# Optimization experiments

Measured on AMD Instinct MI355X. Metric: run time of the kernel, lower is better.

The kernel has to match this reference:

```python
import jax, jax.numpy as jnp
import numpy as np

N = 50000
E = 1000000
WIDTH = 64
DEPTH = 4


def setup_inputs() -> dict:
    key = jax.random.key(0)
    ks = jax.random.split(key, 6)
    x = jax.random.normal(ks[0], (N, 5), dtype=jnp.float32)
    edge_index = jax.random.randint(ks[1], (2, E), 0, N, dtype=jnp.int32)
    edge_attr = jax.random.normal(ks[2], (E, 3), dtype=jnp.float32)
    w1 = jax.random.normal(ks[3], (3, WIDTH), dtype=jnp.float32) / jnp.sqrt(3.0)
    b1 = jnp.zeros((WIDTH,), jnp.float32)
    w2 = jax.random.normal(ks[4], (WIDTH, 1), dtype=jnp.float32) / jnp.sqrt(float(WIDTH))
    b2 = jnp.zeros((1,), jnp.float32)
    root = jax.random.normal(ks[5], (1, 1), dtype=jnp.float32)
    bias = jnp.zeros((1,), jnp.float32)
    return dict(x=x, edge_index=edge_index, edge_attr=edge_attr,
                w1=w1, b1=b1, w2=w2, b2=b2, root=root, bias=bias)


def reference(x, edge_index, edge_attr, w1, b1, w2, b2, root, bias):
    # h: scalar node feature, column 2 of data.x -> [N, 1]
    h = x[:, 2:3]
    src, dst = edge_index[0], edge_index[1]  # messages flow src -> dst

    # Per-edge 1x1 weight from the edge MLP (depends only on edge_attr,
    # identical for all depth iterations since the conv is shared).
    w_e = jax.nn.relu(edge_attr @ w1 + b1) @ w2 + b2  # [E, 1]

    # Mean aggregation: precompute in-degree of each target node.
    deg = jax.ops.segment_sum(jnp.ones((E,), jnp.float32), dst, num_segments=N)
    inv_deg = jnp.where(deg > 0, 1.0 / jnp.maximum(deg, 1.0), 0.0)[:, None]  # [N, 1]

    for _ in range(DEPTH):
        msg = h[src] * w_e                                        # gather + per-edge weight, [E, 1]
        agg = jax.ops.segment_sum(msg, dst, num_segments=N) * inv_deg  # scatter-mean, [N, 1]
        h = jax.nn.relu(agg + h @ root + bias)                    # root transform + bias + ReLU
    return h
```

## Files before the change

### kernel.cpp

```cpp
#include <hip/hip_runtime.h>

#define NN 50000
#define NE 1000000
#define NBK 196
#define EPB 1024
#define PB 977
#define ESTRIDE 5632
#define RK 12

__global__ void init_fixed(const float* __restrict__ x, float* __restrict__ h,
                           int* __restrict__ cursor, int* __restrict__ sBeg,
                           int* __restrict__ sLim) {
    int i = blockIdx.x * 256 + threadIdx.x;
    if (i < NN) h[i] = x[5 * i + 2];
    if (i < NBK) {
        cursor[i] = i * ESTRIDE;
        sBeg[i]   = i * ESTRIDE;
        sLim[i]   = (i + 1) * ESTRIDE;
    }
}

__global__ void bucket_count(const int* __restrict__ dst, int* __restrict__ bcnt,
                             const float* __restrict__ x, float* __restrict__ h) {
    __shared__ int hist[NBK];
    int t = threadIdx.x;
    if (t < NBK) hist[t] = 0;
    __syncthreads();
    int gid = blockIdx.x * 256 + t;
    if (gid < NN) h[gid] = x[5 * gid + 2];
#pragma unroll
    for (int j = 0; j < 4; ++j) {
        int e = blockIdx.x * EPB + j * 256 + t;
        if (e < NE) atomicAdd(&hist[dst[e] >> 8], 1);
    }
    __syncthreads();
    if (t < NBK && hist[t]) atomicAdd(&bcnt[t], hist[t]);
}

__global__ void bucket_scan(const int* __restrict__ bcnt,
                            int* __restrict__ sBeg,
                            int* __restrict__ cursor,
                            int* __restrict__ sLim) {
    __shared__ int part[256];
    int t = threadIdx.x;
    int v = (t < NBK) ? ((bcnt[t] + 1) & ~1) : 0;
    part[t] = v;
    __syncthreads();
    for (int off = 1; off < 256; off <<= 1) {
        int x = part[t];
        int add = (t >= off) ? part[t - off] : 0;
        __syncthreads();
        part[t] = x + add;
        __syncthreads();
    }
    if (t < NBK) {
        int excl = part[t] - v;
        sBeg[t] = excl;
        cursor[t] = excl;
        sLim[t] = 0x7FFFFFFF;
    }
}

__global__ void place_kernel(const float* __restrict__ ea,
                             const int* __restrict__ src,
                             const int* __restrict__ dst,
                             const float* __restrict__ w1,
                             const float* __restrict__ b1,
                             const float* __restrict__ w2,
                             const float* __restrict__ b2,
                             const int* __restrict__ sLim,
                             int* __restrict__ cursor,
                             uint2* __restrict__ es,
                             int dumpbase) {
    __shared__ float sw1[192];
    __shared__ float sb1[64];
    __shared__ float sw2[64];
    __shared__ float sce[EPB];
    __shared__ int hist[NBK];
    __shared__ int hbase[NBK];
    int t = threadIdx.x;
    if (t < 192) sw1[t] = w1[t];
    if (t < 64) { sb1[t] = b1[t]; sw2[t] = w2[t]; }
    if (t < NBK) hist[t] = 0;
    __syncthreads();

    int r[4], dd[4];
#pragma unroll
    for (int j = 0; j < 4; ++j) {
        int e = blockIdx.x * EPB + j * 256 + t;
        dd[j] = -1;
        if (e < NE) {
            float a0 = ea[3 * e + 0];
            float a1 = ea[3 * e + 1];
            float a2 = ea[3 * e + 2];
            float c0 = b2[0], c1 = 0.f, c2 = 0.f, c3 = 0.f;
#pragma unroll
            for (int k = 0; k < 64; k += 4) {
                float h0 = fmaf(a0, sw1[k+0], fmaf(a1, sw1[64+k+0], fmaf(a2, sw1[128+k+0], sb1[k+0])));
                float h1 = fmaf(a0, sw1[k+1], fmaf(a1, sw1[64+k+1], fmaf(a2, sw1[128+k+1], sb1[k+1])));
                float h2 = fmaf(a0, sw1[k+2], fmaf(a1, sw1[64+k+2], fmaf(a2, sw1[128+k+2], sb1[k+2])));
                float h3 = fmaf(a0, sw1[k+3], fmaf(a1, sw1[64+k+3], fmaf(a2, sw1[128+k+3], sb1[k+3])));
                c0 = fmaf(fmaxf(h0, 0.f), sw2[k+0], c0);
                c1 = fmaf(fmaxf(h1, 0.f), sw2[k+1], c1);
                c2 = fmaf(fmaxf(h2, 0.f), sw2[k+2], c2);
                c3 = fmaf(fmaxf(h3, 0.f), sw2[k+3], c3);
            }
            sce[j * 256 + t] = (c0 + c1) + (c2 + c3);
            int d = dst[e];
            dd[j] = d;
            r[j] = atomicAdd(&hist[d >> 8], 1);
        }
    }
    __syncthreads();
    if (t < NBK) { int hv = hist[t]; if (hv) hbase[t] = atomicAdd(&cursor[t], hv); }
    __syncthreads();
#pragma unroll
    for (int j = 0; j < 4; ++j) {
        int e = blockIdx.x * EPB + j * 256 + t;
        if (e < NE) {
            int d = dd[j];
            int b = d >> 8;
            int pos = hbase[b] + r[j];
            if (pos >= sLim[b]) pos = dumpbase + (t & 63);
            unsigned pack = (unsigned)src[e] | ((unsigned)(d & 255) << 17);
            es[pos] = make_uint2(pack, __float_as_uint(sce[j * 256 + t]));
        }
    }
}

__global__ void round1_slice(const int* __restrict__ sBeg,
                             const int* __restrict__ sEnd,
                             const int* __restrict__ sLim,
                             const uint2* __restrict__ es,
                             const float* __restrict__ hold,
                             float* __restrict__ aggS,
                             int* __restrict__ degS) {
    __shared__ float lagg[256];
    __shared__ int ldeg[256];
    int t = threadIdx.x;
    int b = blockIdx.x / RK, c = blockIdx.x % RK;
    lagg[t] = 0.f;
    ldeg[t] = 0;
    __syncthreads();
    int s0 = sBeg[b];
    int s1 = sEnd[b];
    { int cap = sLim[b]; if (s1 > cap) s1 = cap; }
    const uint4* es4 = (const uint4*)es;
    for (int p = s0 + (c * 256 + t) * 2; p < s1; p += RK * 512) {
        uint4 v = es4[p >> 1];
        {
            int sidx = v.x & 0x1FFFF;
            int dl = (v.x >> 17) & 255;
            atomicAdd(&lagg[dl], hold[sidx] * __uint_as_float(v.y));
            atomicAdd(&ldeg[dl], 1);
        }
        if (p + 1 < s1) {
            int sidx = v.z & 0x1FFFF;
            int dl = (v.z >> 17) & 255;
            atomicAdd(&lagg[dl], hold[sidx] * __uint_as_float(v.w));
            atomicAdd(&ldeg[dl], 1);
        }
    }
    __syncthreads();
    int node = b * 256 + t;
    if (node < NN) {
        aggS[c * NN + node] = lagg[t];
        degS[c * NN + node] = ldeg[t];
    }
}

__global__ void round_slice(const int* __restrict__ sBeg,
                            const int* __restrict__ sEnd,
                            const int* __restrict__ sLim,
                            const uint2* __restrict__ es,
                            const float* __restrict__ hold,
                            float* __restrict__ aggS) {
    __shared__ float lagg[256];
    int t = threadIdx.x;
    int b = blockIdx.x / RK, c = blockIdx.x % RK;
    lagg[t] = 0.f;
    __syncthreads();
    int s0 = sBeg[b];
    int s1 = sEnd[b];
    { int cap = sLim[b]; if (s1 > cap) s1 = cap; }
    const uint4* es4 = (const uint4*)es;
    for (int p = s0 + (c * 256 + t) * 2; p < s1; p += RK * 512) {
        uint4 v = es4[p >> 1];
        {
            int sidx = v.x & 0x1FFFF;
            int dl = (v.x >> 17) & 255;
            atomicAdd(&lagg[dl], hold[sidx] * __uint_as_float(v.y));
        }
        if (p + 1 < s1) {
            int sidx = v.z & 0x1FFFF;
            int dl = (v.z >> 17) & 255;
            atomicAdd(&lagg[dl], hold[sidx] * __uint_as_float(v.w));
        }
    }
    __syncthreads();
    int node = b * 256 + t;
    if (node < NN) aggS[c * NN + node] = lagg[t];
}

__global__ void update1(const int* __restrict__ degS,
                        const float* __restrict__ aggS,
                        float* __restrict__ invdeg,
                        const float* __restrict__ hold,
                        float* __restrict__ hnew,
                        const float* __restrict__ root,
                        const float* __restrict__ bias) {
    int i = blockIdx.x * blockDim.x + threadIdx.x;
    if (i >= NN) return;
    int d = 0;
    float a = 0.f;
#pragma unroll
    for (int c = 0; c < RK; ++c) {
        a += aggS[c * NN + i];
        d += degS[c * NN + i];
    }
    float inv = (d > 0) ? (1.0f / (float)d) : 0.f;
    invdeg[i] = inv;
    hnew[i] = fmaxf(fmaf(hold[i], root[0], fmaf(a, inv, bias[0])), 0.f);
}

__global__ void update_kernel(const float* __restrict__ aggS,
                              const float* __restrict__ invdeg,
                              const float* __restrict__ hold,
                              float* __restrict__ hnew,
                              const float* __restrict__ root,
                              const float* __restrict__ bias) {
    int i = blockIdx.x * blockDim.x + threadIdx.x;
    if (i >= NN) return;
    float a = 0.f;
#pragma unroll
    for (int c = 0; c < RK; ++c) a += aggS[c * NN + i];
    hnew[i] = fmaxf(fmaf(hold[i], root[0], fmaf(a, invdeg[i], bias[0])), 0.f);
}


extern "C" void kernel_launch(void* const* d_in, const int* in_sizes, int n_in,
                              void* d_out, int out_size, void* d_ws, size_t ws_size,
                              hipStream_t stream) {
    const float* x    = (const float*)d_in[0];
    const int*   ei   = (const int*)d_in[1];
    const float* ea   = (const float*)d_in[2];
    const float* w1   = (const float*)d_in[3];
    const float* b1   = (const float*)d_in[4];
    const float* w2   = (const float*)d_in[5];
    const float* b2   = (const float*)d_in[6];
    const float* root = (const float*)d_in[7];
    const float* bias = (const float*)d_in[8];

    const int* src = ei;
    const int* dst = ei + NE;
    float* h = (float*)d_out;

    const int BLK = 256;
    const int gN = (NN + BLK - 1) / BLK;
    const int gR = NBK * RK;

    const size_t esFixed = (size_t)NBK * ESTRIDE + 64;
    const size_t needFixed = esFixed * 8
                           + (size_t)(NBK * 3) * 4
                           + (size_t)RK * NN * 4 * 2
                           + (size_t)NN * 4 * 2;

    if (ws_size >= needFixed) {
        uint2* es     = (uint2*)d_ws;
        int*   cursor = (int*)(es + esFixed);
        int*   sBeg   = cursor + NBK;
        int*   sLim   = sBeg + NBK;
        float* aggS   = (float*)(sLim + NBK);
        int*   degS   = (int*)(aggS + (size_t)RK * NN);
        float* invdeg = (float*)(degS + (size_t)RK * NN);
        float* hB     = invdeg + NN;

        init_fixed<<<NBK, BLK, 0, stream>>>(x, h, cursor, sBeg, sLim);
        place_kernel<<<PB, BLK, 0, stream>>>(ea, src, dst, w1, b1, w2, b2,
                                             sLim, cursor, es, (int)(NBK * ESTRIDE));
        round1_slice<<<gR, BLK, 0, stream>>>(sBeg, cursor, sLim, es, h, aggS, degS);
        update1<<<gN, BLK, 0, stream>>>(degS, aggS, invdeg, h, hB, root, bias);
        round_slice<<<gR, BLK, 0, stream>>>(sBeg, cursor, sLim, es, hB, aggS);
        update_kernel<<<gN, BLK, 0, stream>>>(aggS, invdeg, hB, h, root, bias);
        round_slice<<<gR, BLK, 0, stream>>>(sBeg, cursor, sLim, es, h, aggS);
        update_kernel<<<gN, BLK, 0, stream>>>(aggS, invdeg, h, hB, root, bias);
        round_slice<<<gR, BLK, 0, stream>>>(sBeg, cursor, sLim, es, hB, aggS);
        update_kernel<<<gN, BLK, 0, stream>>>(aggS, invdeg, hB, h, root, bias);
    } else {
        uint2* es     = (uint2*)d_ws;
        int*   bcnt   = (int*)(es + NE + NBK);
        int*   cursor = bcnt + NBK;
        int*   sBeg   = cursor + NBK;
        int*   sLim   = sBeg + NBK;
        float* aggS   = (float*)(sLim + NBK);
        int*   degS   = (int*)(aggS + (size_t)RK * NN);
        float* invdeg = (float*)(degS + (size_t)RK * NN);
        float* hB     = invdeg + NN;

        hipMemsetAsync(bcnt, 0, NBK * 4, stream);
        bucket_count<<<PB, BLK, 0, stream>>>(dst, bcnt, x, h);
        bucket_scan<<<1, 256, 0, stream>>>(bcnt, sBeg, cursor, sLim);
        place_kernel<<<PB, BLK, 0, stream>>>(ea, src, dst, w1, b1, w2, b2,
                                             sLim, cursor, es, 0);
        round1_slice<<<gR, BLK, 0, stream>>>(sBeg, cursor, sLim, es, h, aggS, degS);
        update1<<<gN, BLK, 0, stream>>>(degS, aggS, invdeg, h, hB, root, bias);
        round_slice<<<gR, BLK, 0, stream>>>(sBeg, cursor, sLim, es, hB, aggS);
        update_kernel<<<gN, BLK, 0, stream>>>(aggS, invdeg, hB, h, root, bias);
        round_slice<<<gR, BLK, 0, stream>>>(sBeg, cursor, sLim, es, h, aggS);
        update_kernel<<<gN, BLK, 0, stream>>>(aggS, invdeg, h, hB, root, bias);
        round_slice<<<gR, BLK, 0, stream>>>(sBeg, cursor, sLim, es, hB, aggS);
        update_kernel<<<gN, BLK, 0, stream>>>(aggS, invdeg, hB, h, root, bias);
    }
}
```

Measured before the change: 163.3 us.

## Fuse per-round scatter and node update into one 1024-thread block per bucket

Each round previously split every 256-node bucket across 12 blocks, wrote 12 partial aggregates to global memory, and then ran a separate update kernel to reduce them. Now one 1024-thread block handles a whole bucket, reduces in shared memory and applies the mean, root and ReLU update directly. This removes the partial-sum buffers and the four update launches. The cost is far fewer blocks (196 vs 2352), so parallelism is lower and there is more shared-atomic contention per block. It also keeps src and the edge weight in registers in place_kernel instead of reloading src and staging the weight through shared memory.

```diff
diff --git a/kernel.cpp b/kernel.cpp
--- a/kernel.cpp
+++ b/kernel.cpp
@@ -6,7 +6,6 @@
 #define EPB 1024
 #define PB 977
 #define ESTRIDE 5632
-#define RK 12
 
 __global__ void init_fixed(const float* __restrict__ x, float* __restrict__ h,
                            int* __restrict__ cursor, int* __restrict__ sBeg,
@@ -75,7 +74,6 @@
     __shared__ float sw1[192];
     __shared__ float sb1[64];
     __shared__ float sw2[64];
-    __shared__ float sce[EPB];
     __shared__ int hist[NBK];
     __shared__ int hbase[NBK];
     int t = threadIdx.x;
@@ -84,7 +82,8 @@
     if (t < NBK) hist[t] = 0;
     __syncthreads();
 
-    int r[4], dd[4];
+    int r[4], dd[4], ss[4];
+    float ce[4];
 #pragma unroll
     for (int j = 0; j < 4; ++j) {
         int e = blockIdx.x * EPB + j * 256 + t;
@@ -105,7 +104,8 @@
                 c2 = fmaf(fmaxf(h2, 0.f), sw2[k+2], c2);
                 c3 = fmaf(fmaxf(h3, 0.f), sw2[k+3], c3);
             }
-            sce[j * 256 + t] = (c0 + c1) + (c2 + c3);
+            ce[j] = (c0 + c1) + (c2 + c3);
+            ss[j] = src[e];
             int d = dst[e];
             dd[j] = d;
             r[j] = atomicAdd(&hist[d >> 8], 1);
@@ -122,119 +122,64 @@
             int b = d >> 8;
             int pos = hbase[b] + r[j];
             if (pos >= sLim[b]) pos = dumpbase + (t & 63);
-            unsigned pack = (unsigned)src[e] | ((unsigned)(d & 255) << 17);
-            es[pos] = make_uint2(pack, __float_as_uint(sce[j * 256 + t]));
-        }
-    }
-}
-
-__global__ void round1_slice(const int* __restrict__ sBeg,
-                             const int* __restrict__ sEnd,
-                             const int* __restrict__ sLim,
-                             const uint2* __restrict__ es,
-                             const float* __restrict__ hold,
-                             float* __restrict__ aggS,
-                             int* __restrict__ degS) {
+            unsigned pack = (unsigned)ss[j] | ((unsigned)(d & 255) << 17);
+            es[pos] = make_uint2(pack, __float_as_uint(ce[j]));
+        }
+    }
+}
+
+template<int FIRST>
+__global__ __launch_bounds__(1024)
+void round_fused(const int* __restrict__ sBeg,
+                 const int* __restrict__ sEnd,
+                 const int* __restrict__ sLim,
+                 const uint2* __restrict__ es,
+                 const float* __restrict__ hold,
+                 float* __restrict__ hnew,
+                 float* __restrict__ invdeg,
+                 const float* __restrict__ root,
+                 const float* __restrict__ bias) {
     __shared__ float lagg[256];
     __shared__ int ldeg[256];
     int t = threadIdx.x;
-    int b = blockIdx.x / RK, c = blockIdx.x % RK;
-    lagg[t] = 0.f;
-    ldeg[t] = 0;
+    int b = blockIdx.x;
+    if (t < 256) { lagg[t] = 0.f; if (FIRST) ldeg[t] = 0; }
     __syncthreads();
     int s0 = sBeg[b];
     int s1 = sEnd[b];
     { int cap = sLim[b]; if (s1 > cap) s1 = cap; }
     const uint4* es4 = (const uint4*)es;
-    for (int p = s0 + (c * 256 + t) * 2; p < s1; p += RK * 512) {
+    for (int p = s0 + t * 2; p < s1; p += 2048) {
         uint4 v = es4[p >> 1];
         {
             int sidx = v.x & 0x1FFFF;
             int dl = (v.x >> 17) & 255;
             atomicAdd(&lagg[dl], hold[sidx] * __uint_as_float(v.y));
-            atomicAdd(&ldeg[dl], 1);
+            if (FIRST) atomicAdd(&ldeg[dl], 1);
         }
         if (p + 1 < s1) {
             int sidx = v.z & 0x1FFFF;
             int dl = (v.z >> 17) & 255;
             atomicAdd(&lagg[dl], hold[sidx] * __uint_as_float(v.w));
-            atomicAdd(&ldeg[dl], 1);
-        }
-    }
-    __syncthreads();
-    int node = b * 256 + t;
-    if (node < NN) {
-        aggS[c * NN + node] = lagg[t];
-        degS[c * NN + node] = ldeg[t];
-    }
-}
-
-__global__ void round_slice(const int* __restrict__ sBeg,
-                            const int* __restrict__ sEnd,
-                            const int* __restrict__ sLim,
-                            const uint2* __restrict__ es,
-                            const float* __restrict__ hold,
-                            float* __restrict__ aggS) {
-    __shared__ float lagg[256];
-    int t = threadIdx.x;
-    int b = blockIdx.x / RK, c = blockIdx.x % RK;
-    lagg[t] = 0.f;
-    __syncthreads();
-    int s0 = sBeg[b];
-    int s1 = sEnd[b];
-    { int cap = sLim[b]; if (s1 > cap) s1 = cap; }
-    const uint4* es4 = (const uint4*)es;
-    for (int p = s0 + (c * 256 + t) * 2; p < s1; p += RK * 512) {
-        uint4 v = es4[p >> 1];
-        {
-            int sidx = v.x & 0x1FFFF;
-            int dl = (v.x >> 17) & 255;
-            atomicAdd(&lagg[dl], hold[sidx] * __uint_as_float(v.y));
-        }
-        if (p + 1 < s1) {
-            int sidx = v.z & 0x1FFFF;
-            int dl = (v.z >> 17) & 255;
-            atomicAdd(&lagg[dl], hold[sidx] * __uint_as_float(v.w));
-        }
-    }
-    __syncthreads();
-    int node = b * 256 + t;
-    if (node < NN) aggS[c * NN + node] = lagg[t];
-}
-
-__global__ void update1(const int* __restrict__ degS,
-                        const float* __restrict__ aggS,
-                        float* __restrict__ invdeg,
-                        const float* __restrict__ hold,
-                        float* __restrict__ hnew,
-                        const float* __restrict__ root,
-                        const float* __restrict__ bias) {
-    int i = blockIdx.x * blockDim.x + threadIdx.x;
-    if (i >= NN) return;
-    int d = 0;
-    float a = 0.f;
-#pragma unroll
-    for (int c = 0; c < RK; ++c) {
-        a += aggS[c * NN + i];
-        d += degS[c * NN + i];
-    }
-    float inv = (d > 0) ? (1.0f / (float)d) : 0.f;
-    invdeg[i] = inv;
-    hnew[i] = fmaxf(fmaf(hold[i], root[0], fmaf(a, inv, bias[0])), 0.f);
-}
-
-__global__ void update_kernel(const float* __restrict__ aggS,
-                              const float* __restrict__ invdeg,
-                              const float* __restrict__ hold,
-                              float* __restrict__ hnew,
-                              const float* __restrict__ root,
-                              const float* __restrict__ bias) {
-    int i = blockIdx.x * blockDim.x + threadIdx.x;
-    if (i >= NN) return;
-    float a = 0.f;
-#pragma unroll
-    for (int c = 0; c < RK; ++c) a += aggS[c * NN + i];
-    hnew[i] = fmaxf(fmaf(hold[i], root[0], fmaf(a, invdeg[i], bias[0])), 0.f);
+            if (FIRST) atomicAdd(&ldeg[dl], 1);
+        }
+    }
+    __syncthreads();
+    if (t < 256) {
+        int node = b * 256 + t;
+        if (node < NN) {
+            float inv;
+            if (FIRST) {
+                int d = ldeg[t];
+                inv = (d > 0) ? (1.0f / (float)d) : 0.f;
+                invdeg[node] = inv;
+            } else {
+                inv = invdeg[node];
+            }
+            float a = lagg[t];
+            hnew[node] = fmaxf(fmaf(hold[node], root[0], fmaf(a, inv, bias[0])), 0.f);
+        }
+    }
 }
 
 
@@ -256,13 +201,10 @@
     float* h = (float*)d_out;
 
     const int BLK = 256;
-    const int gN = (NN + BLK - 1) / BLK;
-    const int gR = NBK * RK;
 
     const size_t esFixed = (size_t)NBK * ESTRIDE + 64;
     const size_t needFixed = esFixed * 8
                            + (size_t)(NBK * 3) * 4
-                           + (size_t)RK * NN * 4 * 2
                            + (size_t)NN * 4 * 2;
 
     if (ws_size >= needFixed) {
@@ -270,31 +212,23 @@
         int*   cursor = (int*)(es + esFixed);
         int*   sBeg   = cursor + NBK;
         int*   sLim   = sBeg + NBK;
-        float* aggS   = (float*)(sLim + NBK);
-        int*   degS   = (int*)(aggS + (size_t)RK * NN);
-        float* invdeg = (float*)(degS + (size_t)RK * NN);
+        float* invdeg = (float*)(sLim + NBK);
         float* hB     = invdeg + NN;
 
         init_fixed<<<NBK, BLK, 0, stream>>>(x, h, cursor, sBeg, sLim);
         place_kernel<<<PB, BLK, 0, stream>>>(ea, src, dst, w1, b1, w2, b2,
                                              sLim, cursor, es, (int)(NBK * ESTRIDE));
-        round1_slice<<<gR, BLK, 0, stream>>>(sBeg, cursor, sLim, es, h, aggS, degS);
-        update1<<<gN, BLK, 0, stream>>>(degS, aggS, invdeg, h, hB, root, bias);
-        round_slice<<<gR, BLK, 0, stream>>>(sBeg, cursor, sLim, es, hB, aggS);
-        update_kernel<<<gN, BLK, 0, stream>>>(aggS, invdeg, hB, h, root, bias);
-        round_slice<<<gR, BLK, 0, stream>>>(sBeg, cursor, sLim, es, h, aggS);
-        update_kernel<<<gN, BLK, 0, stream>>>(aggS, invdeg, h, hB, root, bias);
-        round_slice<<<gR, BLK, 0, stream>>>(sBeg, cursor, sLim, es, hB, aggS);
-        update_kernel<<<gN, BLK, 0, stream>>>(aggS, invdeg, hB, h, root, bias);
+        round_fused<1><<<NBK, 1024, 0, stream>>>(sBeg, cursor, sLim, es, h,  hB, invdeg, root, bias);
+        round_fused<0><<<NBK, 1024, 0, stream>>>(sBeg, cursor, sLim, es, hB, h,  invdeg, root, bias);
+        round_fused<0><<<NBK, 1024, 0, stream>>>(sBeg, cursor, sLim, es, h,  hB, invdeg, root, bias);
+        round_fused<0><<<NBK, 1024, 0, stream>>>(sBeg, cursor, sLim, es, hB, h,  invdeg, root, bias);
     } else {
         uint2* es     = (uint2*)d_ws;
         int*   bcnt   = (int*)(es + NE + NBK);
         int*   cursor = bcnt + NBK;
         int*   sBeg   = cursor + NBK;
         int*   sLim   = sBeg + NBK;
-        float* aggS   = (float*)(sLim + NBK);
-        int*   degS   = (int*)(aggS + (size_t)RK * NN);
-        float* invdeg = (float*)(degS + (size_t)RK * NN);
+        float* invdeg = (float*)(sLim + NBK);
         float* hB     = invdeg + NN;
 
         hipMemsetAsync(bcnt, 0, NBK * 4, stream);
@@ -302,13 +236,9 @@
         bucket_scan<<<1, 256, 0, stream>>>(bcnt, sBeg, cursor, sLim);
         place_kernel<<<PB, BLK, 0, stream>>>(ea, src, dst, w1, b1, w2, b2,
                                              sLim, cursor, es, 0);
-        round1_slice<<<gR, BLK, 0, stream>>>(sBeg, cursor, sLim, es, h, aggS, degS);
-        update1<<<gN, BLK, 0, stream>>>(degS, aggS, invdeg, h, hB, root, bias);
-        round_slice<<<gR, BLK, 0, stream>>>(sBeg, cursor, sLim, es, hB, aggS);
-        update_kernel<<<gN, BLK, 0, stream>>>(aggS, invdeg, hB, h, root, bias);
-        round_slice<<<gR, BLK, 0, stream>>>(sBeg, cursor, sLim, es, h, aggS);
-        update_kernel<<<gN, BLK, 0, stream>>>(aggS, invdeg, h, hB, root, bias);
-        round_slice<<<gR, BLK, 0, stream>>>(sBeg, cursor, sLim, es, hB, aggS);
-        update_kernel<<<gN, BLK, 0, stream>>>(aggS, invdeg, hB, h, root, bias);
-    }
-}
+        round_fused<1><<<NBK, 1024, 0, stream>>>(sBeg, cursor, sLim, es, h,  hB, invdeg, root, bias);
+        round_fused<0><<<NBK, 1024, 0, stream>>>(sBeg, cursor, sLim, es, hB, h,  invdeg, root, bias);
+        round_fused<0><<<NBK, 1024, 0, stream>>>(sBeg, cursor, sLim, es, h,  hB, invdeg, root, bias);
+        round_fused<0><<<NBK, 1024, 0, stream>>>(sBeg, cursor, sLim, es, hB, h,  invdeg, root, bias);
+    }
+}
```

Result: faster. 151.3 us (-7.4%).
